# Optimization experiments

Hardware: AMD Instinct MI355X
Metric: run time of the kernel (lower is better)

Reference implementation:

```python
import jax, jax.numpy as jnp
import numpy as np

DIM = 256

def setup_inputs() -> dict:
    key = jax.random.key(0)
    ks = jax.random.split(key, 7)
    B, S, D = 8, 4096, DIM
    scale = 1.0 / np.sqrt(D)
    x = jax.random.normal(ks[0], (B, S, D), dtype=jnp.float32)
    # torch Linear: y = x @ W.T + b, W is [out, in]
    Wq = jax.random.normal(ks[1], (D, D), dtype=jnp.float32) * scale
    Wk = jax.random.normal(ks[2], (D, D), dtype=jnp.float32) * scale
    Wv = jax.random.normal(ks[3], (D, D), dtype=jnp.float32) * scale
    bq = jax.random.normal(ks[4], (D,), dtype=jnp.float32) * 0.01
    bk = jax.random.normal(ks[5], (D,), dtype=jnp.float32) * 0.01
    bv = jax.random.normal(ks[6], (D,), dtype=jnp.float32) * 0.01
    return {"x": x, "Wq": Wq, "bq": bq, "Wk": Wk, "bk": bk, "Wv": Wv, "bv": bv}

def reference(x, Wq, bq, Wk, bk, Wv, bv):
    D = x.shape[-1]
    scale = D ** -0.5
    q = jnp.einsum('bsd,ed->bse', x, Wq) + bq  # [B,S,D]
    k = jnp.einsum('bsd,ed->bse', x, Wk) + bk
    v = jnp.einsum('bsd,ed->bse', x, Wv) + bv
    attn = jnp.einsum('bqd,bkd->bqk', q, k) * scale  # [B,S,S]
    attn = jax.nn.softmax(attn, axis=-1)
    return x + jnp.einsum('bqk,bkd->bqd', attn, v)
```

## Files before the change

### kernel.cpp

```cpp
#include <hip/hip_runtime.h>
#include <hip/hip_bf16.h>

typedef __attribute__((ext_vector_type(8))) short bf16x8;
typedef __attribute__((ext_vector_type(4))) float f32x4;
typedef __attribute__((ext_vector_type(16))) float f32x16;

#define MFMA16(a, b, c) __builtin_amdgcn_mfma_f32_16x16x32_bf16(a, b, c, 0, 0, 0)
#define MFMA32(a, b, c) __builtin_amdgcn_mfma_f32_32x32x16_bf16(a, b, c, 0, 0, 0)

__device__ __forceinline__ short f2bf(float f) {
    union { __hip_bfloat16 h; short s; } u;
    u.h = __float2bfloat16(f);
    return u.s;
}

__device__ __forceinline__ bf16x8 cvt8(const float* __restrict__ p) {
    f32x4 a = *reinterpret_cast<const f32x4*>(p);
    f32x4 b = *reinterpret_cast<const f32x4*>(p + 4);
    bf16x8 r;
    r[0] = f2bf(a[0]); r[1] = f2bf(a[1]); r[2] = f2bf(a[2]); r[3] = f2bf(a[3]);
    r[4] = f2bf(b[0]); r[5] = f2bf(b[1]); r[6] = f2bf(b[2]); r[7] = f2bf(b[3]);
    return r;
}

typedef __attribute__((address_space(1))) const unsigned int g_u32;
typedef __attribute__((address_space(3))) unsigned int l_u32;
__device__ __forceinline__ void gld16(const void* g, void* l) {
    __builtin_amdgcn_global_load_lds((g_u32*)(g), (l_u32*)(l), 16, 0, 0);
}

__global__ void wcvt_kernel(const float* __restrict__ Wq, const float* __restrict__ Wk,
                            const float* __restrict__ Wv, short* __restrict__ Wb)
{
    int t = blockIdx.x * 256 + threadIdx.x;
    int idx = t * 8;
    const float* src = idx < 65536 ? Wq + idx
                     : (idx < 131072 ? Wk + (idx - 65536) : Wv + (idx - 131072));
    *reinterpret_cast<bf16x8*>(Wb + idx) = cvt8(src);
}

__global__ __launch_bounds__(256, 2) void qkv_kernel(
    const float* __restrict__ x, const short* __restrict__ Wb,
    const float* __restrict__ bq, const float* __restrict__ bk, const float* __restrict__ bv,
    short* __restrict__ qo, short* __restrict__ ko, short* __restrict__ vto)
{
    const int wave = threadIdx.x >> 6, lane = threadIdx.x & 63;
    const int l31 = lane & 31, h = lane >> 5;
    const int row0 = blockIdx.x * 128;
    const int wrow = row0 + wave * 32;

    bf16x8 af[16];
    const float* __restrict__ xr = x + (size_t)(wrow + l31) * 256 + h * 8;
#pragma unroll
    for (int kc = 0; kc < 16; ++kc) af[kc] = cvt8(xr + kc * 16);

    __shared__ short tile[128][264];

    for (int proj = 0; proj < 3; ++proj) {
        const short* __restrict__ W = Wb + proj * 65536;
        const float* __restrict__ bias = proj == 0 ? bq : (proj == 1 ? bk : bv);

        f32x16 acc[8];
#pragma unroll
        for (int df = 0; df < 8; ++df)
#pragma unroll
            for (int e = 0; e < 16; ++e) acc[df][e] = 0.f;

#pragma unroll
        for (int kc = 0; kc < 16; ++kc)
#pragma unroll
            for (int df = 0; df < 8; ++df) {
                bf16x8 bfr = *reinterpret_cast<const bf16x8*>(
                    W + (df * 32 + l31) * 256 + kc * 16 + h * 8);
                acc[df] = MFMA32(af[kc], bfr, acc[df]);
            }

        if (proj < 2) {
            short* __restrict__ dst = proj == 0 ? qo : ko;
#pragma unroll
            for (int df = 0; df < 8; ++df) {
                int col = df * 32 + l31;
                float bv_ = bias[col];
#pragma unroll
                for (int rg = 0; rg < 16; ++rg) {
                    int r = (rg & 3) + 8 * (rg >> 2) + 4 * h;
                    dst[(size_t)(wrow + r) * 256 + col] = f2bf(acc[df][rg] + bv_);
                }
            }
        } else {
#pragma unroll
            for (int df = 0; df < 8; ++df) {
                int col = df * 32 + l31;
                float bv_ = bias[col];
#pragma unroll
                for (int rg = 0; rg < 16; ++rg) {
                    int r = (rg & 3) + 8 * (rg >> 2) + 4 * h;
                    tile[wave * 32 + r][col] = f2bf(acc[df][rg] + bv_);
                }
            }
            __syncthreads();
            int d = threadIdx.x;
            int bb = row0 >> 12, s0 = row0 & 4095;
            short* __restrict__ dst = vto + ((size_t)bb * 256 + d) * 4096 + s0;
#pragma unroll
            for (int i = 0; i < 16; ++i) {
                bf16x8 v;
#pragma unroll
                for (int j = 0; j < 8; ++j) v[j] = tile[i * 8 + j][d];
                *reinterpret_cast<bf16x8*>(dst + i * 8) = v;
            }
        }
    }
}

__global__ __launch_bounds__(512, 2) void attn_kernel(
    const short* __restrict__ q, const short* __restrict__ k,
    const short* __restrict__ vt, const float* __restrict__ x,
    float* __restrict__ out)
{
    const int id = blockIdx.x;
    const int b = id & 7, qt = id >> 3;
    const int tid = threadIdx.x;
    const int wave = tid >> 6, lane = tid & 63;
    const int l15 = lane & 15, l4 = lane >> 4;
    const int qrow0 = qt * 128 + wave * 16;

    const short* __restrict__ qb = q  + (size_t)b * 4096 * 256;
    const short* __restrict__ kb = k  + (size_t)b * 4096 * 256;
    const short* __restrict__ vb = vt + (size_t)b * 256 * 4096;

    __shared__ short smem[65536];
    __shared__ short plds[8][16][72];
    short (*pw)[72] = plds[wave];

    bf16x8 qf[8];
    const short* __restrict__ qr = qb + (size_t)(qrow0 + l15) * 256 + l4 * 8;
#pragma unroll
    for (int kc = 0; kc < 8; ++kc)
        qf[kc] = *reinterpret_cast<const bf16x8*>(qr + kc * 32);

    f32x4 o[16];
#pragma unroll
    for (int df = 0; df < 16; ++df) { f32x4 z = {0.f,0.f,0.f,0.f}; o[df] = z; }

    float ls[4] = {0.f, 0.f, 0.f, 0.f};
    const float cs = 0.0625f * 1.44269504f;

#define STAGE(T, B)                                                            \
  { _Pragma("unroll")                                                          \
    for (int i = 0; i < 8; ++i) {                                              \
        int c = i * 512 + tid;                                                 \
        int ss = c & 63;                                                       \
        const short* src;                                                      \
        if (c < 2048) {                                                        \
            int nf = c >> 9, kc = (c >> 6) & 7;                                \
            src = kb + (size_t)((T) * 64 + nf * 16 + (ss & 15)) * 256          \
                     + kc * 32 + (ss >> 4) * 8;                                \
        } else {                                                               \
            int df = (c >> 7) & 15, kc2 = (c >> 6) & 1;                        \
            src = vb + (size_t)(df * 16 + (ss & 15)) * 4096 + (T) * 64         \
                     + kc2 * 32 + (ss >> 4) * 8;                               \
        }                                                                      \
        gld16(src, &smem[((B) * 4096 + c) * 8]);                               \
    } }

    STAGE(0, 0);
    __syncthreads();

    for (int t = 0; t < 64; ++t) {
        const int buf = t & 1;
        if (t < 63) STAGE(t + 1, buf ^ 1);

        const short* __restrict__ kb2 = smem + (size_t)buf * 32768;
        const short* __restrict__ vb2 = kb2 + 16384;

        f32x4 sacc[4];
#pragma unroll
        for (int nf = 0; nf < 4; ++nf) { f32x4 z = {0.f,0.f,0.f,0.f}; sacc[nf] = z; }
#pragma unroll
        for (int nf = 0; nf < 4; ++nf)
#pragma unroll
            for (int kc = 0; kc < 8; ++kc) {
                bf16x8 kf = *reinterpret_cast<const bf16x8*>(
                    kb2 + (nf * 512 + kc * 64 + lane) * 8);
                sacc[nf] = MFMA16(qf[kc], kf, sacc[nf]);
            }

#pragma unroll
        for (int nf = 0; nf < 4; ++nf)
#pragma unroll
            for (int r = 0; r < 4; ++r) {
                float p = exp2f(sacc[nf][r] * cs);
                ls[r] += p;
                pw[l4 * 4 + r][nf * 16 + l15] = f2bf(p);
            }
        bf16x8 pf0 = *reinterpret_cast<const bf16x8*>(&pw[l15][l4 * 8]);
        bf16x8 pf1 = *reinterpret_cast<const bf16x8*>(&pw[l15][32 + l4 * 8]);

#pragma unroll
        for (int df = 0; df < 16; ++df) {
            bf16x8 v0 = *reinterpret_cast<const bf16x8*>(
                vb2 + (df * 128 + lane) * 8);
            bf16x8 v1 = *reinterpret_cast<const bf16x8*>(
                vb2 + (df * 128 + 64 + lane) * 8);
            o[df] = MFMA16(pf0, v0, o[df]);
            o[df] = MFMA16(pf1, v1, o[df]);
        }

        __syncthreads();
    }

    float inv[4];
#pragma unroll
    for (int r = 0; r < 4; ++r) {
        float v = ls[r];
#pragma unroll
        for (int d = 1; d < 16; d <<= 1) v += __shfl_xor(v, d);
        inv[r] = 1.0f / v;
    }
#pragma unroll
    for (int r = 0; r < 4; ++r) {
        size_t row = (size_t)b * 4096 + qrow0 + l4 * 4 + r;
#pragma unroll
        for (int df = 0; df < 16; ++df) {
            int col = df * 16 + l15;
            out[row * 256 + col] = o[df][r] * inv[r] + x[row * 256 + col];
        }
    }
#undef STAGE
}

extern "C" void kernel_launch(void* const* d_in, const int* in_sizes, int n_in,
                              void* d_out, int out_size, void* d_ws, size_t ws_size,
                              hipStream_t stream) {
    const float* x  = (const float*)d_in[0];
    const float* Wq = (const float*)d_in[1];
    const float* bq = (const float*)d_in[2];
    const float* Wk = (const float*)d_in[3];
    const float* bk = (const float*)d_in[4];
    const float* Wv = (const float*)d_in[5];
    const float* bv = (const float*)d_in[6];
    float* out = (float*)d_out;

    char* ws = (char*)d_ws;
    short* qb  = (short*)ws;
    short* kb  = (short*)(ws + (size_t)16 * 1024 * 1024);
    short* vtb = (short*)(ws + (size_t)32 * 1024 * 1024);
    short* Wb  = (short*)d_out;

    wcvt_kernel<<<96, 256, 0, stream>>>(Wq, Wk, Wv, Wb);

    qkv_kernel<<<256, 256, 0, stream>>>(x, Wb, bq, bk, bv, qb, kb, vtb);

    attn_kernel<<<256, 512, 0, stream>>>(qb, kb, vtb, x, out);
}
```

Before: 331.7 us.

## Split key tile across wave halves with 32-row query groups and LDS reduction

Each wave now processes 32 query rows (two 16-row groups) against half of each 64-key tile, and the two wave halves split the keys. Every K and V fragment read from LDS now feeds two MFMAs, which halves LDS read traffic per MFMA. The two halves' partial outputs and row sums are combined through shared memory at the end. In exchange, each wave holds twice as many accumulators, which raises register pressure, and the final step adds an LDS exchange plus extra barriers.

```diff
diff --git a/kernel.cpp b/kernel.cpp
--- a/kernel.cpp
+++ b/kernel.cpp
@@ -123,43 +123,55 @@
     const int tid = threadIdx.x;
     const int wave = tid >> 6, lane = tid & 63;
     const int l15 = lane & 15, l4 = lane >> 4;
-    const int qrow0 = qt * 128 + wave * 16;
+    const int qg = wave & 3, hh = wave >> 2;
+    const int qrow0 = qt * 128 + qg * 32;
 
     const short* __restrict__ qb = q  + (size_t)b * 4096 * 256;
     const short* __restrict__ kb = k  + (size_t)b * 4096 * 256;
     const short* __restrict__ vb = vt + (size_t)b * 256 * 4096;
 
     __shared__ short smem[65536];
-    __shared__ short plds[8][16][72];
-    short (*pw)[72] = plds[wave];
-
-    bf16x8 qf[8];
-    const short* __restrict__ qr = qb + (size_t)(qrow0 + l15) * 256 + l4 * 8;
-#pragma unroll
-    for (int kc = 0; kc < 8; ++kc)
-        qf[kc] = *reinterpret_cast<const bf16x8*>(qr + kc * 32);
-
-    f32x4 o[16];
-#pragma unroll
-    for (int df = 0; df < 16; ++df) { f32x4 z = {0.f,0.f,0.f,0.f}; o[df] = z; }
-
-    float ls[4] = {0.f, 0.f, 0.f, 0.f};
+    __shared__ short plds[8][2][16][40];
+    short (*pw)[16][40] = plds[wave];
+
+    bf16x8 qf[2][8];
+#pragma unroll
+    for (int rg = 0; rg < 2; ++rg) {
+        const short* __restrict__ qr =
+            qb + (size_t)(qrow0 + rg * 16 + l15) * 256 + l4 * 8;
+#pragma unroll
+        for (int kc = 0; kc < 8; ++kc)
+            qf[rg][kc] = *reinterpret_cast<const bf16x8*>(qr + kc * 32);
+    }
+
+    f32x4 o[2][16];
+#pragma unroll
+    for (int rg = 0; rg < 2; ++rg)
+#pragma unroll
+        for (int df = 0; df < 16; ++df) { f32x4 z = {0.f,0.f,0.f,0.f}; o[rg][df] = z; }
+
+    float ls[2][4];
+#pragma unroll
+    for (int rg = 0; rg < 2; ++rg)
+#pragma unroll
+        for (int r = 0; r < 4; ++r) ls[rg][r] = 0.f;
+
     const float cs = 0.0625f * 1.44269504f;
 
 #define STAGE(T, B)                                                            \
   { _Pragma("unroll")                                                          \
     for (int i = 0; i < 8; ++i) {                                              \
         int c = i * 512 + tid;                                                 \
-        int ss = c & 63;                                                       \
         const short* src;                                                      \
         if (c < 2048) {                                                        \
-            int nf = c >> 9, kc = (c >> 6) & 7;                                \
-            src = kb + (size_t)((T) * 64 + nf * 16 + (ss & 15)) * 256          \
-                     + kc * 32 + (ss >> 4) * 8;                                \
+            int hh_ = c >> 10, nf = (c >> 9) & 1, kc = (c >> 6) & 7, l = c & 63;\
+            src = kb + (size_t)((T) * 64 + hh_ * 32 + nf * 16 + (l & 15)) * 256\
+                     + kc * 32 + (l >> 4) * 8;                                 \
         } else {                                                               \
-            int df = (c >> 7) & 15, kc2 = (c >> 6) & 1;                        \
-            src = vb + (size_t)(df * 16 + (ss & 15)) * 4096 + (T) * 64         \
-                     + kc2 * 32 + (ss >> 4) * 8;                               \
+            int s = c & 2047;                                                  \
+            int hh_ = s >> 10, df = (s >> 6) & 15, l = s & 63;                 \
+            src = vb + (size_t)(df * 16 + (l & 15)) * 4096 + (T) * 64          \
+                     + hh_ * 32 + (l >> 4) * 8;                                \
         }                                                                      \
         gld16(src, &smem[((B) * 4096 + c) * 8]);                               \
     } }
@@ -171,60 +183,94 @@
         const int buf = t & 1;
         if (t < 63) STAGE(t + 1, buf ^ 1);
 
-        const short* __restrict__ kb2 = smem + (size_t)buf * 32768;
-        const short* __restrict__ vb2 = kb2 + 16384;
-
-        f32x4 sacc[4];
-#pragma unroll
-        for (int nf = 0; nf < 4; ++nf) { f32x4 z = {0.f,0.f,0.f,0.f}; sacc[nf] = z; }
-#pragma unroll
-        for (int nf = 0; nf < 4; ++nf)
+        const short* __restrict__ kbase = smem + ((size_t)buf * 4096 + hh * 1024) * 8;
+        const short* __restrict__ vbase = smem + ((size_t)buf * 4096 + 2048 + hh * 1024) * 8;
+
+        f32x4 sacc[2][2];
+#pragma unroll
+        for (int rg = 0; rg < 2; ++rg)
+#pragma unroll
+            for (int nf = 0; nf < 2; ++nf) { f32x4 z = {0.f,0.f,0.f,0.f}; sacc[rg][nf] = z; }
+#pragma unroll
+        for (int nf = 0; nf < 2; ++nf)
 #pragma unroll
             for (int kc = 0; kc < 8; ++kc) {
                 bf16x8 kf = *reinterpret_cast<const bf16x8*>(
-                    kb2 + (nf * 512 + kc * 64 + lane) * 8);
-                sacc[nf] = MFMA16(qf[kc], kf, sacc[nf]);
-            }
-
-#pragma unroll
-        for (int nf = 0; nf < 4; ++nf)
-#pragma unroll
-            for (int r = 0; r < 4; ++r) {
-                float p = exp2f(sacc[nf][r] * cs);
-                ls[r] += p;
-                pw[l4 * 4 + r][nf * 16 + l15] = f2bf(p);
-            }
-        bf16x8 pf0 = *reinterpret_cast<const bf16x8*>(&pw[l15][l4 * 8]);
-        bf16x8 pf1 = *reinterpret_cast<const bf16x8*>(&pw[l15][32 + l4 * 8]);
+                    kbase + (nf * 512 + kc * 64 + lane) * 8);
+                sacc[0][nf] = MFMA16(qf[0][kc], kf, sacc[0][nf]);
+                sacc[1][nf] = MFMA16(qf[1][kc], kf, sacc[1][nf]);
+            }
+
+#pragma unroll
+        for (int rg = 0; rg < 2; ++rg)
+#pragma unroll
+            for (int nf = 0; nf < 2; ++nf)
+#pragma unroll
+                for (int r = 0; r < 4; ++r) {
+                    float p = exp2f(sacc[rg][nf][r] * cs);
+                    ls[rg][r] += p;
+                    pw[rg][l4 * 4 + r][nf * 16 + l15] = f2bf(p);
+                }
+        bf16x8 pf0 = *reinterpret_cast<const bf16x8*>(&pw[0][l15][l4 * 8]);
+        bf16x8 pf1 = *reinterpret_cast<const bf16x8*>(&pw[1][l15][l4 * 8]);
 
 #pragma unroll
         for (int df = 0; df < 16; ++df) {
-            bf16x8 v0 = *reinterpret_cast<const bf16x8*>(
-                vb2 + (df * 128 + lane) * 8);
-            bf16x8 v1 = *reinterpret_cast<const bf16x8*>(
-                vb2 + (df * 128 + 64 + lane) * 8);
-            o[df] = MFMA16(pf0, v0, o[df]);
-            o[df] = MFMA16(pf1, v1, o[df]);
+            bf16x8 vf = *reinterpret_cast<const bf16x8*>(
+                vbase + (df * 64 + lane) * 8);
+            o[0][df] = MFMA16(pf0, vf, o[0][df]);
+            o[1][df] = MFMA16(pf1, vf, o[1][df]);
         }
 
         __syncthreads();
     }
 
-    float inv[4];
-#pragma unroll
-    for (int r = 0; r < 4; ++r) {
-        float v = ls[r];
-#pragma unroll
-        for (int d = 1; d < 16; d <<= 1) v += __shfl_xor(v, d);
-        inv[r] = 1.0f / v;
-    }
-#pragma unroll
-    for (int r = 0; r < 4; ++r) {
-        size_t row = (size_t)b * 4096 + qrow0 + l4 * 4 + r;
-#pragma unroll
-        for (int df = 0; df < 16; ++df) {
-            int col = df * 16 + l15;
-            out[row * 256 + col] = o[df][r] * inv[r] + x[row * 256 + col];
+#pragma unroll
+    for (int rg = 0; rg < 2; ++rg)
+#pragma unroll
+        for (int r = 0; r < 4; ++r) {
+            float v = ls[rg][r];
+#pragma unroll
+            for (int d = 1; d < 16; d <<= 1) v += __shfl_xor(v, d);
+            ls[rg][r] = v;
+        }
+
+    f32x4* __restrict__ fo = (f32x4*)smem;
+    float* __restrict__ fl = (float*)plds;
+
+    __syncthreads();
+
+    if (hh == 1) {
+#pragma unroll
+        for (int rg = 0; rg < 2; ++rg) {
+#pragma unroll
+            for (int df = 0; df < 16; ++df)
+                fo[((qg * 2 + rg) * 16 + df) * 64 + lane] = o[rg][df];
+#pragma unroll
+            for (int r = 0; r < 4; ++r)
+                fl[((qg * 2 + rg) * 4 + r) * 64 + lane] = ls[rg][r];
+        }
+    }
+    __syncthreads();
+
+    if (hh == 0) {
+#pragma unroll
+        for (int rg = 0; rg < 2; ++rg) {
+            float inv[4];
+#pragma unroll
+            for (int r = 0; r < 4; ++r)
+                inv[r] = 1.0f / (ls[rg][r] + fl[((qg * 2 + rg) * 4 + r) * 64 + lane]);
+#pragma unroll
+            for (int df = 0; df < 16; ++df) {
+                f32x4 od = fo[((qg * 2 + rg) * 16 + df) * 64 + lane];
+                int col = df * 16 + l15;
+#pragma unroll
+                for (int r = 0; r < 4; ++r) {
+                    size_t row = (size_t)b * 4096 + qrow0 + rg * 16 + l4 * 4 + r;
+                    out[row * 256 + col] =
+                        (o[rg][df][r] + od[r]) * inv[r] + x[row * 256 + col];
+                }
+            }
         }
     }
 #undef STAGE
```

New measurement: 339.4 us. 2.3% more time.
